# Optimization experiments

Measured on AMD Instinct MI355X. Metric: run time of the kernel, lower is better.

The kernel has to match this reference:

```python
import jax, jax.numpy as jnp
import numpy as np

# canonical SMPL kinematic tree (24 joints)
PARENTS = [-1, 0, 0, 0, 1, 2, 3, 4, 5, 6, 7, 8, 9, 9, 9, 12, 13, 14, 16, 17, 18, 19, 20, 21]
B, V, J, NB = 512, 6890, 24, 10


def setup_inputs() -> dict:
    key = jax.random.key(0)
    ks = jax.random.split(key, 9)
    betas = jax.random.normal(ks[0], (B, NB), jnp.float32)
    body_pose = 0.3 * jax.random.normal(ks[1], (B, (J - 1) * 3), jnp.float32)
    global_orient = 0.3 * jax.random.normal(ks[2], (B, 3), jnp.float32)
    transl = jax.random.normal(ks[3], (B, 3), jnp.float32)
    v_template = jax.random.normal(ks[4], (V, 3), jnp.float32)
    shapedirs = 0.01 * jax.random.normal(ks[5], (V, 3, NB), jnp.float32)
    posedirs = 0.01 * jax.random.normal(ks[6], (9 * (J - 1), V * 3), jnp.float32)
    J_regressor = jax.nn.softmax(4.0 * jax.random.normal(ks[7], (J, V), jnp.float32), axis=-1)
    lbs_weights = jax.nn.softmax(4.0 * jax.random.normal(ks[8], (V, J), jnp.float32), axis=-1)
    return {"betas": betas, "body_pose": body_pose, "global_orient": global_orient,
            "transl": transl, "v_template": v_template, "shapedirs": shapedirs,
            "posedirs": posedirs, "J_regressor": J_regressor, "lbs_weights": lbs_weights}


def rodrigues(rot_vecs):
    # rot_vecs: [B, J, 3] axis-angle -> [B, J, 3, 3] rotation matrices
    angle = jnp.linalg.norm(rot_vecs + 1e-8, axis=-1, keepdims=True)  # [B,J,1]
    axis = rot_vecs / angle
    s = jnp.sin(angle)[..., None]
    c = jnp.cos(angle)[..., None]
    x, y, z = axis[..., 0], axis[..., 1], axis[..., 2]
    zeros = jnp.zeros_like(x)
    K = jnp.stack([zeros, -z, y, z, zeros, -x, -y, x, zeros], axis=-1)
    K = K.reshape(rot_vecs.shape[:-1] + (3, 3))
    ident = jnp.eye(3, dtype=rot_vecs.dtype)
    return ident + s * K + (1.0 - c) * (K @ K)


def lbs(betas, full_pose, v_template, shapedirs, posedirs, J_regressor, lbs_weights):
    b = betas.shape[0]
    dtype = betas.dtype
    # shape blendshapes: [B,V,3]
    v_shaped = v_template[None] + jnp.einsum('bl,vkl->bvk', betas, shapedirs)
    # rest joints: [B,J,3]
    Jrest = jnp.einsum('jv,bvk->bjk', J_regressor, v_shaped)
    # pose -> rotation matrices [B,J,3,3]
    rot_mats = rodrigues(full_pose.reshape(b, -1, 3))
    ident = jnp.eye(3, dtype=dtype)
    pose_feature = (rot_mats[:, 1:] - ident).reshape(b, -1)  # [B,207]
    v_posed = v_shaped + (pose_feature @ posedirs).reshape(b, V, 3)
    # relative joint locations along the tree
    parents = np.asarray(PARENTS)
    rel_J = Jrest.at[:, 1:].add(-Jrest[:, parents[1:]])
    # local 4x4 transforms [B,J,4,4]
    T34 = jnp.concatenate([rot_mats, rel_J[..., None]], axis=-1)  # [B,J,3,4]
    bottom = jnp.broadcast_to(jnp.array([0, 0, 0, 1], dtype=dtype), (b, J, 1, 4))
    T_local = jnp.concatenate([T34, bottom], axis=-2)
    # sequential chain over the fixed 24-joint kinematic tree
    chain = [T_local[:, 0]]
    for i in range(1, J):
        chain.append(chain[parents[i]] @ T_local[:, i])
    Tg = jnp.stack(chain, axis=1)  # [B,J,4,4]
    posed_joints = Tg[:, :, :3, 3]
    # remove rest-pose joint contribution: A = Tg - pack(Tg[:, :, :3, :3] @ Jrest)
    corr = jnp.einsum('bjmn,bjn->bjm', Tg[:, :, :3, :3], Jrest)  # [B,J,3]
    corr4 = jnp.concatenate([corr, jnp.zeros((b, J, 1), dtype=dtype)], axis=-1)
    A = Tg.at[..., 3].add(-corr4)
    # skinning: per-vertex transform [B,V,4,4]
    T = jnp.einsum('vj,bjmn->bvmn', lbs_weights, A)
    v_h = jnp.concatenate([v_posed, jnp.ones((b, V, 1), dtype=dtype)], axis=-1)
    verts = jnp.einsum('bvmn,bvn->bvm', T, v_h)[..., :3]
    return verts, posed_joints


def reference(betas, body_pose, global_orient, transl, v_template, shapedirs,
              posedirs, J_regressor, lbs_weights):
    full_pose = jnp.concatenate([global_orient, body_pose], axis=1)  # [B,72]
    vertices, joints = lbs(betas, full_pose, v_template, shapedirs, posedirs,
                           J_regressor, lbs_weights)
    vertices = vertices + transl[:, None, :]
    joints = joints + transl[:, None, :]
    return vertices, joints
```

## Files before the change

### kernel.cpp

```cpp
#include <hip/hip_runtime.h>
#include <math.h>

#define B_    512
#define V_    6890
#define J_    24
#define NB_   10
#define K_    207
#define KPAD  224
#define NCOL  20670
#define TV    32
#define TC    96
#define CPAD  20736
#define NCVT  2268
#define NPOSE 128

typedef __attribute__((ext_vector_type(8))) __bf16 bf16x8;
typedef __attribute__((ext_vector_type(4))) float  f32x4;

__constant__ int c_par[24] = {-1,0,0,0,1,2,3,4,5,6,7,8,9,9,9,12,13,14,16,17,18,19,20,21};
__constant__ int c_lev[24] = { 0,1,1,1,2,2,2,3,3,3,4,4,4,4,4, 5, 5, 5, 6, 6, 7, 7, 8, 8};

__device__ __forceinline__ unsigned short f2bf(float x) {
    union { float f; unsigned u; } v; v.f = x;
    unsigned r = (v.u + 0x7FFFu + ((v.u >> 16) & 1u)) >> 16;
    return (unsigned short)r;
}
__device__ __forceinline__ float bf2f(unsigned short h) {
    union { unsigned u; float f; } v; v.u = (unsigned)h << 16;
    return v.f;
}
__device__ __forceinline__ void wsync() {
    asm volatile("s_waitcnt lgkmcnt(0)" ::: "memory");
}

__global__ __launch_bounds__(256) void k_jreg(const float* __restrict__ Jreg,
                                              const float* __restrict__ vt,
                                              const float* __restrict__ sd,
                                              float* __restrict__ JS,
                                              float* __restrict__ JT)
{
    const int j = blockIdx.x / 3, k = blockIdx.x % 3;
    const int tid = threadIdx.x;
    float acc[11];
#pragma unroll
    for (int i = 0; i < 11; ++i) acc[i] = 0.f;

    for (int v = tid; v < V_; v += 256) {
        const float r = Jreg[j * V_ + v];
        acc[0] = fmaf(r, vt[v * 3 + k], acc[0]);
        const float* s = &sd[(v * 3 + k) * NB_];
#pragma unroll
        for (int l = 0; l < NB_; ++l) acc[1 + l] = fmaf(r, s[l], acc[1 + l]);
    }

    __shared__ float red[4][11];
    const int lane = tid & 63, w = tid >> 6;
#pragma unroll
    for (int i = 0; i < 11; ++i) {
        float a = acc[i];
        for (int off = 32; off; off >>= 1) a += __shfl_xor(a, off, 64);
        acc[i] = a;
    }
    if (lane == 0) {
#pragma unroll
        for (int i = 0; i < 11; ++i) red[w][i] = acc[i];
    }
    __syncthreads();
    if (tid == 0) {
        for (int i = 0; i < 11; ++i) {
            const float s = red[0][i] + red[1][i] + red[2][i] + red[3][i];
            if (i == 0) JT[j * 3 + k] = s;
            else        JS[(j * 3 + k) * NB_ + (i - 1)] = s;
        }
    }
}

__global__ __launch_bounds__(256) void k_mid(const float* __restrict__ pd,
                                             const float* __restrict__ sd,
                                             const float* __restrict__ betas,
                                             const float* __restrict__ body_pose,
                                             const float* __restrict__ global_orient,
                                             const float* __restrict__ transl,
                                             const float* __restrict__ JS,
                                             const float* __restrict__ JT,
                                             unsigned short* __restrict__ pdT,
                                             unsigned short* __restrict__ Atout,
                                             unsigned short* __restrict__ pfout,
                                             float* __restrict__ joints_out,
                                             int do_cvt)
{
    const int tid = threadIdx.x;
    const int bx  = blockIdx.x;

    if (bx < NCVT) {
        if (!do_cvt) return;
        const int c  = (bx % 324) * 64 + (tid & 63);
        const int kq = (bx / 324) * 4 + (tid >> 6);
        unsigned short u[8];
#pragma unroll
        for (int e = 0; e < 8; ++e) {
            const int k = kq * 8 + e;
            float x = 0.f;
            if (c < NCOL) {
                if (k < K_)            x = pd[(size_t)k * NCOL + c];
                else if (k < K_ + NB_) x = sd[(size_t)c * NB_ + (k - K_)];
            }
            u[e] = f2bf(x);
        }
        *reinterpret_cast<uint4*>(&pdT[(size_t)c * KPAD + kq * 8]) =
            *reinterpret_cast<const uint4*>(u);
        return;
    }

    const int wv   = tid >> 6;
    const int j    = tid & 63;
    const int b    = (bx - NCVT) * 4 + wv;

    __shared__ float sR[4][24][9];
    __shared__ float sJ[4][24][3];
    __shared__ float sTl[4][24][12];
    __shared__ float sTg[4][24][12];

    if (j < 24) {
        float rx, ry, rz;
        if (j == 0) {
            rx = global_orient[b * 3 + 0];
            ry = global_orient[b * 3 + 1];
            rz = global_orient[b * 3 + 2];
        } else {
            const float* p = &body_pose[b * 69 + (j - 1) * 3];
            rx = p[0]; ry = p[1]; rz = p[2];
        }
        const float ax = rx + 1e-8f, ay = ry + 1e-8f, az = rz + 1e-8f;
        const float angle = sqrtf(ax * ax + ay * ay + az * az);
        const float inv = 1.f / angle;
        const float x = rx * inv, y = ry * inv, z = rz * inv;
        const float s = sinf(angle), c = cosf(angle), t = 1.f - c;

        float R[9];
        R[0] = 1.f - t * (y * y + z * z);
        R[1] = -s * z + t * x * y;
        R[2] =  s * y + t * x * z;
        R[3] =  s * z + t * x * y;
        R[4] = 1.f - t * (x * x + z * z);
        R[5] = -s * x + t * y * z;
        R[6] = -s * y + t * x * z;
        R[7] =  s * x + t * y * z;
        R[8] = 1.f - t * (x * x + y * y);

#pragma unroll
        for (int e = 0; e < 9; ++e) sR[wv][j][e] = R[e];

        if (j >= 1) {
#pragma unroll
            for (int e = 0; e < 9; ++e) {
                const float id = (e == 0 || e == 4 || e == 8) ? 1.f : 0.f;
                pfout[b * KPAD + (j - 1) * 9 + e] = f2bf(R[e] - id);
            }
        }
#pragma unroll
        for (int k = 0; k < 3; ++k) {
            float jr = JT[j * 3 + k];
#pragma unroll
            for (int l = 0; l < NB_; ++l)
                jr = fmaf(betas[b * NB_ + l], JS[(j * 3 + k) * NB_ + l], jr);
            sJ[wv][j][k] = jr;
        }
    }
    if (j < KPAD - K_) {
        const float val = (j < NB_) ? betas[b * NB_ + j] : 0.f;
        pfout[b * KPAD + K_ + j] = f2bf(val);
    }
    wsync();

    if (j < 24) {
        const int p = c_par[j];
        float t0 = sJ[wv][j][0], t1 = sJ[wv][j][1], t2 = sJ[wv][j][2];
        if (j > 0) { t0 -= sJ[wv][p][0]; t1 -= sJ[wv][p][1]; t2 -= sJ[wv][p][2]; }
        sTl[wv][j][0] = sR[wv][j][0]; sTl[wv][j][1] = sR[wv][j][1];
        sTl[wv][j][2] = sR[wv][j][2]; sTl[wv][j][3] = t0;
        sTl[wv][j][4] = sR[wv][j][3]; sTl[wv][j][5] = sR[wv][j][4];
        sTl[wv][j][6] = sR[wv][j][5]; sTl[wv][j][7] = t1;
        sTl[wv][j][8] = sR[wv][j][6]; sTl[wv][j][9] = sR[wv][j][7];
        sTl[wv][j][10] = sR[wv][j][8]; sTl[wv][j][11] = t2;
    }
    wsync();

    if (j == 0) {
#pragma unroll
        for (int e = 0; e < 12; ++e) sTg[wv][0][e] = sTl[wv][0][e];
    }
    wsync();

    for (int lev = 1; lev <= 8; ++lev) {
        if (j < 24 && c_lev[j] == lev) {
            const int p = c_par[j];
            float o[12];
#pragma unroll
            for (int r = 0; r < 3; ++r) {
#pragma unroll
                for (int c = 0; c < 4; ++c) {
                    float v = (c == 3) ? sTg[wv][p][r * 4 + 3] : 0.f;
#pragma unroll
                    for (int m = 0; m < 3; ++m)
                        v = fmaf(sTg[wv][p][r * 4 + m], sTl[wv][j][m * 4 + c], v);
                    o[r * 4 + c] = v;
                }
            }
#pragma unroll
            for (int e = 0; e < 12; ++e) sTg[wv][j][e] = o[e];
        }
        wsync();
    }

    if (j < 24) {
        float corr[3];
#pragma unroll
        for (int r = 0; r < 3; ++r)
            corr[r] = sTg[wv][j][r * 4 + 0] * sJ[wv][j][0]
                    + sTg[wv][j][r * 4 + 1] * sJ[wv][j][1]
                    + sTg[wv][j][r * 4 + 2] * sJ[wv][j][2];

#pragma unroll
        for (int r = 0; r < 3; ++r) {
            float row[4];
            row[0] = sTg[wv][j][r * 4 + 0];
            row[1] = sTg[wv][j][r * 4 + 1];
            row[2] = sTg[wv][j][r * 4 + 2];
            row[3] = sTg[wv][j][r * 4 + 3] - corr[r] + transl[b * 3 + r];
#pragma unroll
            for (int cc = 0; cc < 4; ++cc) {
                const float val = row[cc];
                const unsigned short hi = f2bf(val);
                const unsigned short lo = f2bf(val - bf2f(hi));
                const size_t base = ((size_t)b * 16 + r * 4 + cc) * 64;
                Atout[base + j]      = hi;
                Atout[base + 32 + j] = lo;
            }
        }
#pragma unroll
        for (int k = 0; k < 3; ++k)
            joints_out[(b * 24 + j) * 3 + k] = sTg[wv][j][k * 4 + 3] + transl[b * 3 + k];
    }
    for (int idx = j; idx < 1024; idx += 64) {
        const int e = idx >> 6, jj = idx & 63;
        if (e >= 12 || (jj & 31) >= 24)
            Atout[((size_t)b * 16 + e) * 64 + jj] = 0;
    }
}

template<bool PRE>
__global__ __launch_bounds__(256, 6) void k_verts(
    const float* __restrict__ v_template,
    const float* __restrict__ posedirs,
    const float* __restrict__ shapedirs,
    const unsigned short* __restrict__ pdT,
    const float* __restrict__ lbs_weights,
    const unsigned short* __restrict__ pf,
    const unsigned short* __restrict__ At,
    float* __restrict__ out)
{
    __shared__ __align__(16) char smem[15360 + 2048];
    unsigned short* s_pd = (unsigned short*)smem;
    unsigned short* s_w  = (unsigned short*)(smem + 15360);
    float*          s_vp = (float*)smem;

    const int tid = threadIdx.x;
    const int l   = tid & 63;
    const int wv  = tid >> 6;
    const int m   = l & 15;
    const int g   = l >> 4;

    const int lraw  = blockIdx.x;
    const int gl    = (lraw & 7) * 216 + (lraw >> 3);
    const int vtile = gl >> 3;
    const int btile = gl & 7;
    const int vbase = vtile * TV;
    const int bbase = btile * 64;
    const int vb3   = vtile * TC;

    if (tid < 128) {
        const int v  = tid >> 2, jq = tid & 3;
        const int vv = vbase + v;
        const int vc = vv < V_ ? vv : V_ - 1;
        unsigned short u[8];
        if (jq < 3) {
            const float* src = &lbs_weights[vc * 24 + jq * 8];
#pragma unroll
            for (int e = 0; e < 8; ++e) u[e] = f2bf(src[e]);
        } else {
#pragma unroll
            for (int e = 0; e < 8; ++e) u[e] = 0;
        }
        *reinterpret_cast<uint4*>(&s_w[v * 32 + jq * 8]) =
            *reinterpret_cast<const uint4*>(u);
    }

    auto ld_chunk = [&](int kc, int it, uint4& dst) {
        const int idx = it * 256 + tid;
        if (it == 1 && tid >= 128) return;
        const int col = idx >> 2, g4 = idx & 3;
        if (PRE) {
            dst = *reinterpret_cast<const uint4*>(
                &pdT[(size_t)(vb3 + col) * KPAD + kc + g4 * 8]);
        } else {
            unsigned short u[8];
            const int c = vb3 + col;
#pragma unroll
            for (int e = 0; e < 8; ++e) {
                const int k = kc + g4 * 8 + e;
                float x = 0.f;
                if (c < NCOL) {
                    if (k < K_)            x = posedirs[(size_t)k * NCOL + c];
                    else if (k < K_ + NB_) x = shapedirs[(size_t)c * NB_ + (k - K_)];
                }
                u[e] = f2bf(x);
            }
            dst = *reinterpret_cast<const uint4*>(u);
        }
    };
    auto st_chunk = [&](int buf, int it, const uint4& v) {
        const int idx = it * 256 + tid;
        if (it == 1 && tid >= 128) return;
        const int col = idx >> 2, g4 = idx & 3;
        *reinterpret_cast<uint4*>(&s_pd[buf * 3840 + col * 40 + g4 * 8]) = v;
    };

    {
        uint4 t0, t1;
        ld_chunk(0, 0, t0); ld_chunk(0, 1, t1);
        st_chunk(0, 0, t0); st_chunk(0, 1, t1);
    }
    __syncthreads();

    f32x4 acc1[6];
#pragma unroll
    for (int i = 0; i < 6; ++i) acc1[i] = (f32x4){0.f, 0.f, 0.f, 0.f};

    int cur = 0;
#pragma unroll 1
    for (int ck = 0; ck < 7; ++ck) {
        uint4 t0, t1;
        if (ck < 6) {
            ld_chunk((ck + 1) * 32, 0, t0);
            ld_chunk((ck + 1) * 32, 1, t1);
        }
        const bf16x8 af = *reinterpret_cast<const bf16x8*>(
            &pf[(size_t)(bbase + wv * 16 + m) * KPAD + ck * 32 + g * 8]);
        const unsigned short* pb = &s_pd[cur * 3840 + m * 40 + g * 8];
#pragma unroll
        for (int nt = 0; nt < 6; ++nt) {
            const bf16x8 bfr = *reinterpret_cast<const bf16x8*>(&pb[nt * 640]);
            acc1[nt] = __builtin_amdgcn_mfma_f32_16x16x32_bf16(af, bfr, acc1[nt], 0, 0, 0);
        }
        if (ck < 6) {
            st_chunk(cur ^ 1, 0, t0);
            st_chunk(cur ^ 1, 1, t1);
        }
        __syncthreads();
        cur ^= 1;
    }

    bf16x8 wf[2];
#pragma unroll
    for (int nt = 0; nt < 2; ++nt)
        wf[nt] = *reinterpret_cast<const bf16x8*>(&s_w[(nt * 16 + m) * 32 + g * 8]);

    float* vp = &s_vp[wv * 8 * TC];

#pragma unroll 1
    for (int h = 0; h < 2; ++h) {
        if ((g >> 1) == h) {
            const int r4 = (g & 1) * 4;
#pragma unroll
            for (int nt = 0; nt < 6; ++nt) {
                const int c = vb3 + nt * 16 + m;
                const float vtf = (c < NCOL) ? v_template[c] : 0.f;
#pragma unroll
                for (int r = 0; r < 4; ++r)
                    vp[(r4 + r) * TC + nt * 16 + m] = acc1[nt][r] + vtf;
            }
        }
        wsync();

        const int b0 = bbase + wv * 16 + h * 8;
        bf16x8 nhi = *reinterpret_cast<const bf16x8*>(&At[((size_t)b0 * 16 + m) * 64 + g * 8]);
        bf16x8 nlo = *reinterpret_cast<const bf16x8*>(&At[((size_t)b0 * 16 + m) * 64 + 32 + g * 8]);

#pragma unroll 1
        for (int mt8 = 0; mt8 < 8; ++mt8) {
            const bf16x8 ahi = nhi, alo = nlo;
            if (mt8 < 7) {
                const size_t arow = ((size_t)(b0 + mt8 + 1) * 16 + m) * 64;
                nhi = *reinterpret_cast<const bf16x8*>(&At[arow + g * 8]);
                nlo = *reinterpret_cast<const bf16x8*>(&At[arow + 32 + g * 8]);
            }
            const int b = b0 + mt8;
#pragma unroll
            for (int nt = 0; nt < 2; ++nt) {
                f32x4 t = (f32x4){0.f, 0.f, 0.f, 0.f};
                t = __builtin_amdgcn_mfma_f32_16x16x32_bf16(ahi, wf[nt], t, 0, 0, 0);
                t = __builtin_amdgcn_mfma_f32_16x16x32_bf16(alo, wf[nt], t, 0, 0, 0);
                const float vpx = vp[mt8 * TC + nt * 48 + 3 * m + 0];
                const float vpy = vp[mt8 * TC + nt * 48 + 3 * m + 1];
                const float vpz = vp[mt8 * TC + nt * 48 + 3 * m + 2];
                const float o = fmaf(t[0], vpx, fmaf(t[1], vpy, fmaf(t[2], vpz, t[3])));
                const int vv = vbase + nt * 16 + m;
                if (g < 3 && vv < V_)
                    out[((size_t)b * V_ + vv) * 3 + g] = o;
            }
        }
        wsync();
    }
}

extern "C" void kernel_launch(void* const* d_in, const int* in_sizes, int n_in,
                              void* d_out, int out_size, void* d_ws, size_t ws_size,
                              hipStream_t stream)
{
    const float* betas         = (const float*)d_in[0];
    const float* body_pose     = (const float*)d_in[1];
    const float* global_orient = (const float*)d_in[2];
    const float* transl        = (const float*)d_in[3];
    const float* v_template    = (const float*)d_in[4];
    const float* shapedirs     = (const float*)d_in[5];
    const float* posedirs      = (const float*)d_in[6];
    const float* J_regressor   = (const float*)d_in[7];
    const float* lbs_weights   = (const float*)d_in[8];

    float* out = (float*)d_out;
    float* ws  = (float*)d_ws;

    float* JS = ws;
    float* JT = ws + 720;
    unsigned short* pfw = (unsigned short*)(ws + 792);
    unsigned short* Atw = pfw + (size_t)B_ * KPAD;
    unsigned short* pdT = Atw + (size_t)B_ * 16 * 64;

    const size_t needed_pre = 792u * 4 + (size_t)B_ * KPAD * 2
                            + (size_t)B_ * 16 * 64 * 2
                            + (size_t)CPAD * KPAD * 2;
    const bool pre = (ws_size >= needed_pre);

    float* joints = out + (size_t)B_ * V_ * 3;

    k_jreg<<<72, 256, 0, stream>>>(J_regressor, v_template, shapedirs, JS, JT);
    k_mid <<<NCVT + NPOSE, 256, 0, stream>>>(posedirs, shapedirs, betas,
                                             body_pose, global_orient, transl,
                                             JS, JT, pdT, Atw, pfw, joints,
                                             pre ? 1 : 0);
    if (pre) {
        k_verts<true><<<1728, 256, 0, stream>>>(v_template, posedirs, shapedirs,
                                                pdT, lbs_weights, pfw, Atw, out);
    } else {
        k_verts<false><<<1728, 256, 0, stream>>>(v_template, posedirs, shapedirs,
                                                 pdT, lbs_weights, pfw, Atw, out);
    }
}
```

Before: 80.70 us.

## Stage full posedirs K-slab in LDS once and merge jreg into conversion kernel

k_verts now loads the whole 224-deep bf16 posedirs tile for its 96 columns into LDS at once, with a padded stride. This replaces the double-buffered per-chunk loop with its per-step syncthreads, and all A fragments are preloaded into registers. The pose-blend output for all 16 batch rows per wave is staged in one pass, and the skinning loop is fully unrolled with two-deep prefetch of the At rows. The joint-regressor reduction is folded into the conversion kernel as extra blocks, and the pose stage becomes its own kernel. In exchange, the larger LDS footprint and register use drop occupancy from 6 to 3 blocks per CU.

```diff
diff --git a/kernel.cpp b/kernel.cpp
--- a/kernel.cpp
+++ b/kernel.cpp
@@ -12,7 +12,8 @@
 #define TC    96
 #define CPAD  20736
 #define NCVT  2268
-#define NPOSE 128
+#define SPD_STRIDE 232
+#define VP_STRIDE  100
 
 typedef __attribute__((ext_vector_type(8))) __bf16 bf16x8;
 typedef __attribute__((ext_vector_type(4))) float  f32x4;
@@ -33,60 +34,13 @@
     asm volatile("s_waitcnt lgkmcnt(0)" ::: "memory");
 }
 
-__global__ __launch_bounds__(256) void k_jreg(const float* __restrict__ Jreg,
-                                              const float* __restrict__ vt,
-                                              const float* __restrict__ sd,
-                                              float* __restrict__ JS,
-                                              float* __restrict__ JT)
-{
-    const int j = blockIdx.x / 3, k = blockIdx.x % 3;
-    const int tid = threadIdx.x;
-    float acc[11];
-#pragma unroll
-    for (int i = 0; i < 11; ++i) acc[i] = 0.f;
-
-    for (int v = tid; v < V_; v += 256) {
-        const float r = Jreg[j * V_ + v];
-        acc[0] = fmaf(r, vt[v * 3 + k], acc[0]);
-        const float* s = &sd[(v * 3 + k) * NB_];
-#pragma unroll
-        for (int l = 0; l < NB_; ++l) acc[1 + l] = fmaf(r, s[l], acc[1 + l]);
-    }
-
-    __shared__ float red[4][11];
-    const int lane = tid & 63, w = tid >> 6;
-#pragma unroll
-    for (int i = 0; i < 11; ++i) {
-        float a = acc[i];
-        for (int off = 32; off; off >>= 1) a += __shfl_xor(a, off, 64);
-        acc[i] = a;
-    }
-    if (lane == 0) {
-#pragma unroll
-        for (int i = 0; i < 11; ++i) red[w][i] = acc[i];
-    }
-    __syncthreads();
-    if (tid == 0) {
-        for (int i = 0; i < 11; ++i) {
-            const float s = red[0][i] + red[1][i] + red[2][i] + red[3][i];
-            if (i == 0) JT[j * 3 + k] = s;
-            else        JS[(j * 3 + k) * NB_ + (i - 1)] = s;
-        }
-    }
-}
-
-__global__ __launch_bounds__(256) void k_mid(const float* __restrict__ pd,
+__global__ __launch_bounds__(256) void k_pre(const float* __restrict__ pd,
                                              const float* __restrict__ sd,
-                                             const float* __restrict__ betas,
-                                             const float* __restrict__ body_pose,
-                                             const float* __restrict__ global_orient,
-                                             const float* __restrict__ transl,
-                                             const float* __restrict__ JS,
-                                             const float* __restrict__ JT,
+                                             const float* __restrict__ Jreg,
+                                             const float* __restrict__ vt,
                                              unsigned short* __restrict__ pdT,
-                                             unsigned short* __restrict__ Atout,
-                                             unsigned short* __restrict__ pfout,
-                                             float* __restrict__ joints_out,
+                                             float* __restrict__ JS,
+                                             float* __restrict__ JT,
                                              int do_cvt)
 {
     const int tid = threadIdx.x;
@@ -112,9 +66,56 @@
         return;
     }
 
-    const int wv   = tid >> 6;
-    const int j    = tid & 63;
-    const int b    = (bx - NCVT) * 4 + wv;
+    const int jk = bx - NCVT;
+    const int j = jk / 3, k = jk % 3;
+    float acc[11];
+#pragma unroll
+    for (int i = 0; i < 11; ++i) acc[i] = 0.f;
+
+#pragma unroll 4
+    for (int v = tid; v < V_; v += 256) {
+        const float r = Jreg[j * V_ + v];
+        acc[0] = fmaf(r, vt[v * 3 + k], acc[0]);
+        const float* s = &sd[(v * 3 + k) * NB_];
+#pragma unroll
+        for (int l = 0; l < NB_; ++l) acc[1 + l] = fmaf(r, s[l], acc[1 + l]);
+    }
+
+    __shared__ float red[4][11];
+    const int lane = tid & 63, w = tid >> 6;
+#pragma unroll
+    for (int i = 0; i < 11; ++i) {
+        float a = acc[i];
+        for (int off = 32; off; off >>= 1) a += __shfl_xor(a, off, 64);
+        acc[i] = a;
+    }
+    if (lane == 0) {
+#pragma unroll
+        for (int i = 0; i < 11; ++i) red[w][i] = acc[i];
+    }
+    __syncthreads();
+    if (tid == 0) {
+        for (int i = 0; i < 11; ++i) {
+            const float s = red[0][i] + red[1][i] + red[2][i] + red[3][i];
+            if (i == 0) JT[j * 3 + k] = s;
+            else        JS[(j * 3 + k) * NB_ + (i - 1)] = s;
+        }
+    }
+}
+
+__global__ __launch_bounds__(256) void k_pose(const float* __restrict__ betas,
+                                              const float* __restrict__ body_pose,
+                                              const float* __restrict__ global_orient,
+                                              const float* __restrict__ transl,
+                                              const float* __restrict__ JS,
+                                              const float* __restrict__ JT,
+                                              unsigned short* __restrict__ Atout,
+                                              unsigned short* __restrict__ pfout,
+                                              float* __restrict__ joints_out)
+{
+    const int wv   = threadIdx.x >> 6;
+    const int j    = threadIdx.x & 63;
+    const int b    = blockIdx.x * 4 + wv;
 
     __shared__ float sR[4][24][9];
     __shared__ float sJ[4][24][3];
@@ -250,7 +251,7 @@
 }
 
 template<bool PRE>
-__global__ __launch_bounds__(256, 6) void k_verts(
+__global__ __launch_bounds__(256, 3) void k_verts(
     const float* __restrict__ v_template,
     const float* __restrict__ posedirs,
     const float* __restrict__ shapedirs,
@@ -260,9 +261,9 @@
     const unsigned short* __restrict__ At,
     float* __restrict__ out)
 {
-    __shared__ __align__(16) char smem[15360 + 2048];
+    __shared__ __align__(16) char smem[44544 + 2048];
     unsigned short* s_pd = (unsigned short*)smem;
-    unsigned short* s_w  = (unsigned short*)(smem + 15360);
+    unsigned short* s_w  = (unsigned short*)(smem + 44544);
     float*          s_vp = (float*)smem;
 
     const int tid = threadIdx.x;
@@ -296,19 +297,21 @@
             *reinterpret_cast<const uint4*>(u);
     }
 
-    auto ld_chunk = [&](int kc, int it, uint4& dst) {
-        const int idx = it * 256 + tid;
-        if (it == 1 && tid >= 128) return;
-        const int col = idx >> 2, g4 = idx & 3;
+#pragma unroll
+    for (int i = 0; i < 11; ++i) {
+        const int idx = i * 256 + tid;
+        if (i == 10 && tid >= 128) break;
+        const int col = idx / 28, kq = idx % 28;
+        uint4 val;
         if (PRE) {
-            dst = *reinterpret_cast<const uint4*>(
-                &pdT[(size_t)(vb3 + col) * KPAD + kc + g4 * 8]);
+            val = *reinterpret_cast<const uint4*>(
+                &pdT[(size_t)(vb3 + col) * KPAD + kq * 8]);
         } else {
             unsigned short u[8];
             const int c = vb3 + col;
 #pragma unroll
             for (int e = 0; e < 8; ++e) {
-                const int k = kc + g4 * 8 + e;
+                const int k = kq * 8 + e;
                 float x = 0.f;
                 if (c < NCOL) {
                     if (k < K_)            x = posedirs[(size_t)k * NCOL + c];
@@ -316,101 +319,83 @@
                 }
                 u[e] = f2bf(x);
             }
-            dst = *reinterpret_cast<const uint4*>(u);
-        }
-    };
-    auto st_chunk = [&](int buf, int it, const uint4& v) {
-        const int idx = it * 256 + tid;
-        if (it == 1 && tid >= 128) return;
-        const int col = idx >> 2, g4 = idx & 3;
-        *reinterpret_cast<uint4*>(&s_pd[buf * 3840 + col * 40 + g4 * 8]) = v;
-    };
-
-    {
-        uint4 t0, t1;
-        ld_chunk(0, 0, t0); ld_chunk(0, 1, t1);
-        st_chunk(0, 0, t0); st_chunk(0, 1, t1);
-    }
+            val = *reinterpret_cast<const uint4*>(u);
+        }
+        *reinterpret_cast<uint4*>(&s_pd[col * SPD_STRIDE + kq * 8]) = val;
+    }
+
+    bf16x8 af[7];
+#pragma unroll
+    for (int ck = 0; ck < 7; ++ck)
+        af[ck] = *reinterpret_cast<const bf16x8*>(
+            &pf[(size_t)(bbase + wv * 16 + m) * KPAD + ck * 32 + g * 8]);
+
     __syncthreads();
 
     f32x4 acc1[6];
 #pragma unroll
     for (int i = 0; i < 6; ++i) acc1[i] = (f32x4){0.f, 0.f, 0.f, 0.f};
 
-    int cur = 0;
-#pragma unroll 1
+#pragma unroll
     for (int ck = 0; ck < 7; ++ck) {
-        uint4 t0, t1;
-        if (ck < 6) {
-            ld_chunk((ck + 1) * 32, 0, t0);
-            ld_chunk((ck + 1) * 32, 1, t1);
-        }
-        const bf16x8 af = *reinterpret_cast<const bf16x8*>(
-            &pf[(size_t)(bbase + wv * 16 + m) * KPAD + ck * 32 + g * 8]);
-        const unsigned short* pb = &s_pd[cur * 3840 + m * 40 + g * 8];
+        const unsigned short* pb = &s_pd[m * SPD_STRIDE + ck * 32 + g * 8];
 #pragma unroll
         for (int nt = 0; nt < 6; ++nt) {
-            const bf16x8 bfr = *reinterpret_cast<const bf16x8*>(&pb[nt * 640]);
-            acc1[nt] = __builtin_amdgcn_mfma_f32_16x16x32_bf16(af, bfr, acc1[nt], 0, 0, 0);
-        }
-        if (ck < 6) {
-            st_chunk(cur ^ 1, 0, t0);
-            st_chunk(cur ^ 1, 1, t1);
-        }
-        __syncthreads();
-        cur ^= 1;
-    }
+            const bf16x8 bfr = *reinterpret_cast<const bf16x8*>(
+                &pb[nt * 16 * SPD_STRIDE]);
+            acc1[nt] = __builtin_amdgcn_mfma_f32_16x16x32_bf16(af[ck], bfr, acc1[nt], 0, 0, 0);
+        }
+    }
+
+    __syncthreads();
+
+    float* vp = &s_vp[wv * 16 * VP_STRIDE];
+#pragma unroll
+    for (int nt = 0; nt < 6; ++nt) {
+        const int c = vb3 + nt * 16 + m;
+        const float vtf = (c < NCOL) ? v_template[c] : 0.f;
+#pragma unroll
+        for (int r = 0; r < 4; ++r)
+            vp[(g * 4 + r) * VP_STRIDE + nt * 16 + m] = acc1[nt][r] + vtf;
+    }
+    wsync();
 
     bf16x8 wf[2];
 #pragma unroll
     for (int nt = 0; nt < 2; ++nt)
         wf[nt] = *reinterpret_cast<const bf16x8*>(&s_w[(nt * 16 + m) * 32 + g * 8]);
 
-    float* vp = &s_vp[wv * 8 * TC];
-
-#pragma unroll 1
-    for (int h = 0; h < 2; ++h) {
-        if ((g >> 1) == h) {
-            const int r4 = (g & 1) * 4;
-#pragma unroll
-            for (int nt = 0; nt < 6; ++nt) {
-                const int c = vb3 + nt * 16 + m;
-                const float vtf = (c < NCOL) ? v_template[c] : 0.f;
-#pragma unroll
-                for (int r = 0; r < 4; ++r)
-                    vp[(r4 + r) * TC + nt * 16 + m] = acc1[nt][r] + vtf;
-            }
-        }
-        wsync();
-
-        const int b0 = bbase + wv * 16 + h * 8;
-        bf16x8 nhi = *reinterpret_cast<const bf16x8*>(&At[((size_t)b0 * 16 + m) * 64 + g * 8]);
-        bf16x8 nlo = *reinterpret_cast<const bf16x8*>(&At[((size_t)b0 * 16 + m) * 64 + 32 + g * 8]);
-
-#pragma unroll 1
-        for (int mt8 = 0; mt8 < 8; ++mt8) {
-            const bf16x8 ahi = nhi, alo = nlo;
-            if (mt8 < 7) {
-                const size_t arow = ((size_t)(b0 + mt8 + 1) * 16 + m) * 64;
-                nhi = *reinterpret_cast<const bf16x8*>(&At[arow + g * 8]);
-                nlo = *reinterpret_cast<const bf16x8*>(&At[arow + 32 + g * 8]);
-            }
-            const int b = b0 + mt8;
-#pragma unroll
-            for (int nt = 0; nt < 2; ++nt) {
-                f32x4 t = (f32x4){0.f, 0.f, 0.f, 0.f};
-                t = __builtin_amdgcn_mfma_f32_16x16x32_bf16(ahi, wf[nt], t, 0, 0, 0);
-                t = __builtin_amdgcn_mfma_f32_16x16x32_bf16(alo, wf[nt], t, 0, 0, 0);
-                const float vpx = vp[mt8 * TC + nt * 48 + 3 * m + 0];
-                const float vpy = vp[mt8 * TC + nt * 48 + 3 * m + 1];
-                const float vpz = vp[mt8 * TC + nt * 48 + 3 * m + 2];
-                const float o = fmaf(t[0], vpx, fmaf(t[1], vpy, fmaf(t[2], vpz, t[3])));
-                const int vv = vbase + nt * 16 + m;
-                if (g < 3 && vv < V_)
-                    out[((size_t)b * V_ + vv) * 3 + g] = o;
-            }
-        }
-        wsync();
+    const int b0 = bbase + wv * 16;
+    bf16x8 phi[2], plo[2];
+#pragma unroll
+    for (int p = 0; p < 2; ++p) {
+        const size_t arow = ((size_t)(b0 + p) * 16 + m) * 64;
+        phi[p] = *reinterpret_cast<const bf16x8*>(&At[arow + g * 8]);
+        plo[p] = *reinterpret_cast<const bf16x8*>(&At[arow + 32 + g * 8]);
+    }
+
+#pragma unroll
+    for (int mt8 = 0; mt8 < 16; ++mt8) {
+        const bf16x8 ahi = phi[mt8 & 1], alo = plo[mt8 & 1];
+        if (mt8 < 14) {
+            const size_t arow = ((size_t)(b0 + mt8 + 2) * 16 + m) * 64;
+            phi[mt8 & 1] = *reinterpret_cast<const bf16x8*>(&At[arow + g * 8]);
+            plo[mt8 & 1] = *reinterpret_cast<const bf16x8*>(&At[arow + 32 + g * 8]);
+        }
+        const int b = b0 + mt8;
+#pragma unroll
+        for (int nt = 0; nt < 2; ++nt) {
+            f32x4 t = (f32x4){0.f, 0.f, 0.f, 0.f};
+            t = __builtin_amdgcn_mfma_f32_16x16x32_bf16(ahi, wf[nt], t, 0, 0, 0);
+            t = __builtin_amdgcn_mfma_f32_16x16x32_bf16(alo, wf[nt], t, 0, 0, 0);
+            const float vpx = vp[mt8 * VP_STRIDE + nt * 48 + 3 * m + 0];
+            const float vpy = vp[mt8 * VP_STRIDE + nt * 48 + 3 * m + 1];
+            const float vpz = vp[mt8 * VP_STRIDE + nt * 48 + 3 * m + 2];
+            const float o = fmaf(t[0], vpx, fmaf(t[1], vpy, fmaf(t[2], vpz, t[3])));
+            const int vv = vbase + nt * 16 + m;
+            if (g < 3 && vv < V_)
+                out[((size_t)b * V_ + vv) * 3 + g] = o;
+        }
     }
 }
 
@@ -444,11 +429,10 @@
 
     float* joints = out + (size_t)B_ * V_ * 3;
 
-    k_jreg<<<72, 256, 0, stream>>>(J_regressor, v_template, shapedirs, JS, JT);
-    k_mid <<<NCVT + NPOSE, 256, 0, stream>>>(posedirs, shapedirs, betas,
-                                             body_pose, global_orient, transl,
-                                             JS, JT, pdT, Atw, pfw, joints,
-                                             pre ? 1 : 0);
+    k_pre <<<NCVT + 72, 256, 0, stream>>>(posedirs, shapedirs, J_regressor,
+                                          v_template, pdT, JS, JT, pre ? 1 : 0);
+    k_pose<<<B_ / 4, 256, 0, stream>>>(betas, body_pose, global_orient, transl,
+                                       JS, JT, Atw, pfw, joints);
     if (pre) {
         k_verts<true><<<1728, 256, 0, stream>>>(v_template, posedirs, shapedirs,
                                                 pdT, lbs_weights, pfw, Atw, out);
```

Measured after the change: 76.98 us. -4.6%, faster.
